# Kernel optimization log

Hardware: AMD Instinct MI355X
Metric: run time of the kernel (lower is better)

The kernel has to match this reference:

```python
import jax, jax.numpy as jnp
import numpy as np

B, DIN, DP, DOUT, K, N = 4, 64, 3, 64, 16, 8192


def setup_inputs() -> dict:
    key = jax.random.key(0)
    ks = jax.random.split(key, 5)
    features = jax.random.normal(ks[0], (B, DIN, N), dtype=jnp.float32)
    positions = jax.random.normal(ks[1], (B, DP, N), dtype=jnp.float32)
    neighborhoods = jax.random.randint(ks[2], (B, K, N), 0, N, dtype=jnp.int32)
    position_theta = jax.random.normal(ks[3], (DP, DIN, DOUT), dtype=jnp.float32) * 0.05
    position_bias = jnp.zeros((DIN, DOUT), dtype=jnp.float32)
    feature_bias = jnp.zeros((DOUT, 1), dtype=jnp.float32)
    return {
        "features": features,
        "positions": positions,
        "neighborhoods": neighborhoods,
        "position_theta": position_theta,
        "position_bias": position_bias,
        "feature_bias": feature_bias,
    }


def _gather_neighbors(x, idx):
    # x: [D, N], idx: [K, N] -> [D, K, N]
    return x[:, idx]


def reference(features, positions, neighborhoods, position_theta, position_bias, feature_bias):
    # Gather neighbor features/positions: [B, D, K, N]
    fg = jax.vmap(_gather_neighbors)(features, neighborhoods)      # [B, Din, K, N]
    pg = jax.vmap(_gather_neighbors)(positions, neighborhoods)     # [B, Dp,  K, N]
    # Relative positions of neighbors w.r.t. center point
    rel = pg - positions[:, :, None, :]                            # [B, Dp, K, N]
    # Dynamic weight w[b,k,n] = theta . rel + bias, contracted with
    # gathered features and summed over K, without materializing [Din,Dout] per neighbor.
    y = jnp.einsum('pio,bpkn,bikn->bon', position_theta, rel, fg)
    y = y + jnp.einsum('io,bikn->bon', position_bias, fg)
    # feature bias [Dout, 1] broadcasts over [B, Dout, N]
    y = y + feature_bias[None, :, :]
    return y  # [B, Dout, N]; activation=None (linear)
```

## Files before the change

kernel.cpp:

```cpp
#include <hip/hip_runtime.h>

#define NB    4
#define DIN_  64
#define DOUT_ 64
#define KN    16
#define NPT   8192
#define CPAD  264

typedef __attribute__((ext_vector_type(8))) short short8;
typedef __attribute__((ext_vector_type(4))) float v4f;

__device__ __forceinline__ float bf2f(unsigned short u) {
    unsigned int x = ((unsigned int)u) << 16;
    float f; __builtin_memcpy(&f, &x, 4); return f;
}
__device__ __forceinline__ unsigned short f2bf(float f) {
    unsigned int x; __builtin_memcpy(&x, &f, 4);
    x += 0x7fffu + ((x >> 16) & 1u);
    return (unsigned short)(x >> 16);
}

__global__ void k_prep(const float* __restrict__ feat, const float* __restrict__ pos,
                       const float* __restrict__ theta, const float* __restrict__ pbias,
                       unsigned short* __restrict__ ft, float4* __restrict__ pt,
                       unsigned short* __restrict__ tbf) {
    __shared__ float tile[64][65];
    const int bid = blockIdx.x;
    if (bid < 512) {
        int b = bid >> 7, n0 = (bid & 127) << 6;
        int lane = threadIdx.x & 63, w = threadIdx.x >> 6;
#pragma unroll
        for (int r = 0; r < 16; ++r) {
            int i = (r << 2) | w;
            tile[i][lane] = feat[(b*DIN_ + i)*NPT + n0 + lane];
        }
        __syncthreads();
#pragma unroll
        for (int r = 0; r < 16; ++r) {
            int n = (r << 2) | w;
            ft[((size_t)(b*NPT + n0 + n))*DIN_ + lane] = f2bf(tile[lane][n]);
        }
    } else if (bid < 640) {
        int t = (bid - 512)*256 + threadIdx.x;
        int b = t >> 13, n = t & 8191;
        float4 v;
        v.x = pos[(b*3 + 0)*NPT + n];
        v.y = pos[(b*3 + 1)*NPT + n];
        v.z = pos[(b*3 + 2)*NPT + n];
        v.w = 1.0f;
        pt[t] = v;
    } else {
        int e = (bid - 640)*256 + threadIdx.x;
        int o = e >> 5, g = e & 31;
        short8 u;
#pragma unroll
        for (int j = 0; j < 8; ++j) {
            int c = g*8 + j;
            float v = (c < 192) ? theta[c*64 + o] : pbias[(c - 192)*64 + o];
            u[j] = (short)f2bf(v);
        }
        *reinterpret_cast<short8*>(tbf + o*256 + g*8) = u;
    }
}

template<bool USE_WS>
__global__ __launch_bounds__(256, 4) void k_main(
    const float*          __restrict__ feat,
    const float*          __restrict__ pos,
    const int*            __restrict__ nbr,
    const float*          __restrict__ theta,
    const float*          __restrict__ pbias,
    const float*          __restrict__ fbias,
    const unsigned short* __restrict__ ft,
    const float4*         __restrict__ pt,
    const unsigned short* __restrict__ tbf,
    float*                __restrict__ out)
{
    __shared__ __align__(16) unsigned short Xt[32*CPAD];
    __shared__ int    nbs[KN*32];
    __shared__ float4 pcs[32];

    const int tid  = threadIdx.x;
    const int lane = tid & 63;
    const int w    = tid >> 6;
    const int j16  = lane & 15;
    const int pt2  = lane >> 4;

    const int base = blockIdx.x << 5;
    const int b    = base >> 13;
    const int nb0  = base & 8191;

#pragma unroll
    for (int r = 0; r < 2; ++r) {
        int idx = tid + (r << 8);
        int k = idx >> 5, c = idx & 31;
        nbs[idx] = nbr[(b*KN + k)*NPT + nb0 + c];
    }
    if (tid < 128) {
        if (USE_WS) {
            ((float*)pcs)[tid] = ((const float*)(pt + b*NPT + nb0))[tid];
        } else if (tid < 32) {
            int n = nb0 + tid;
            pcs[tid] = make_float4(pos[(b*3+0)*NPT + n], pos[(b*3+1)*NPT + n],
                                   pos[(b*3+2)*NPT + n], 1.0f);
        }
    }
    __syncthreads();

    const unsigned short* ftb = ft + (((size_t)b) << 19);

#pragma unroll
    for (int pass = 0; pass < 2; ++pass) {
        const int q = (w << 3) + (pass << 2) + pt2;
        const float4 pc = pcs[q];
        float acc[4][4];
#pragma unroll
        for (int p = 0; p < 4; ++p)
#pragma unroll
            for (int j = 0; j < 4; ++j) acc[p][j] = 0.f;

#pragma unroll 4
        for (int k = 0; k < KN; ++k) {
            const int id = nbs[(k << 5) + q];
            float4 pg; float f[4];
            if (USE_WS) {
                pg = pt[b*NPT + id];
                ushort4 fr = *reinterpret_cast<const ushort4*>(
                    ftb + (((size_t)id) << 6) + (j16 << 2));
                f[0]=bf2f(fr.x); f[1]=bf2f(fr.y); f[2]=bf2f(fr.z); f[3]=bf2f(fr.w);
            } else {
                pg.x = pos[(b*3+0)*NPT + id];
                pg.y = pos[(b*3+1)*NPT + id];
                pg.z = pos[(b*3+2)*NPT + id];
                pg.w = 1.0f;
#pragma unroll
                for (int j = 0; j < 4; ++j)
                    f[j] = feat[(b*DIN_ + (j16<<2) + j)*NPT + id];
            }
#pragma unroll
            for (int j = 0; j < 4; ++j) {
                acc[0][j] += pg.x * f[j];
                acc[1][j] += pg.y * f[j];
                acc[2][j] += pg.z * f[j];
                acc[3][j] += f[j];
            }
        }
#pragma unroll
        for (int j = 0; j < 4; ++j) {
            acc[0][j] -= pc.x * acc[3][j];
            acc[1][j] -= pc.y * acc[3][j];
            acc[2][j] -= pc.z * acc[3][j];
        }
#pragma unroll
        for (int p = 0; p < 4; ++p) {
            ushort4 pk;
            pk.x = f2bf(acc[p][0]); pk.y = f2bf(acc[p][1]);
            pk.z = f2bf(acc[p][2]); pk.w = f2bf(acc[p][3]);
            *reinterpret_cast<ushort4*>(&Xt[q*CPAD + (p<<6) + (j16<<2)]) = pk;
        }
    }
    __syncthreads();

    const int kg   = pt2;
    const int orow = (w << 4) + j16;
    v4f acc0 = {0.f,0.f,0.f,0.f}, acc1 = {0.f,0.f,0.f,0.f};
#pragma unroll
    for (int ks = 0; ks < 8; ++ks) {
        const int koff = (ks << 5) + (kg << 3);
        short8 a;
        if (USE_WS) {
            a = *reinterpret_cast<const short8*>(tbf + orow*256 + koff);
        } else {
#pragma unroll
            for (int j = 0; j < 8; ++j) {
                int c = koff + j;
                float v = (c < 192) ? theta[c*64 + orow] : pbias[(c - 192)*64 + orow];
                a[j] = (short)f2bf(v);
            }
        }
        short8 b0 = *reinterpret_cast<const short8*>(&Xt[j16*CPAD + koff]);
        short8 b1 = *reinterpret_cast<const short8*>(&Xt[(16 + j16)*CPAD + koff]);
        acc0 = __builtin_amdgcn_mfma_f32_16x16x32_bf16(a, b0, acc0, 0, 0, 0);
        acc1 = __builtin_amdgcn_mfma_f32_16x16x32_bf16(a, b1, acc1, 0, 0, 0);
    }
#pragma unroll
    for (int r = 0; r < 4; ++r) {
        const int o = (w << 4) + (kg << 2) + r;
        const float fb = fbias[o];
        const size_t rowoff = (size_t)(b*DOUT_ + o)*NPT + nb0;
        out[rowoff + j16]      = acc0[r] + fb;
        out[rowoff + 16 + j16] = acc1[r] + fb;
    }
}

extern "C" void kernel_launch(void* const* d_in, const int* in_sizes, int n_in,
                              void* d_out, int out_size, void* d_ws, size_t ws_size,
                              hipStream_t stream) {
    const float* feat  = (const float*)d_in[0];
    const float* pos   = (const float*)d_in[1];
    const int*   nbr   = (const int*)d_in[2];
    const float* theta = (const float*)d_in[3];
    const float* pbias = (const float*)d_in[4];
    const float* fbias = (const float*)d_in[5];
    float* out = (float*)d_out;

    const size_t ft_bytes  = (size_t)NB*NPT*DIN_*2;
    const size_t pt_bytes  = (size_t)NB*NPT*sizeof(float4);
    const size_t tbf_bytes = (size_t)DOUT_*256*2;
    const int n_blocks = (NB*NPT)/32;

    if (ws_size >= ft_bytes + pt_bytes + tbf_bytes) {
        unsigned short* ft  = (unsigned short*)d_ws;
        float4*         pt  = (float4*)((char*)d_ws + ft_bytes);
        unsigned short* tbf = (unsigned short*)((char*)d_ws + ft_bytes + pt_bytes);
        k_prep<<<648, 256, 0, stream>>>(feat, pos, theta, pbias, ft, pt, tbf);
        k_main<true><<<n_blocks, 256, 0, stream>>>(feat, pos, nbr, theta, pbias, fbias,
                                                   ft, pt, tbf, out);
    } else {
        k_main<false><<<n_blocks, 256, 0, stream>>>(feat, pos, nbr, theta, pbias, fbias,
                                                    (const unsigned short*)feat,
                                                    (const float4*)feat,
                                                    (const unsigned short*)feat, out);
    }
}
```

Before: 89.25 us.

## Remap gather phase to one pass with 8 channels per lane and direct index loads

The gather/accumulate phase now gives each lane 8 bf16 channels loaded as one 16-byte short8 instead of 4 channels loaded as 8 bytes. With 8 points per wave, the two-pass loop collapses into a single pass. The neighbor indices and center positions are read straight from global memory rather than staged through shared memory. The K loop is fully unrolled, which drops a __syncthreads and exposes more independent loads, at the cost of more registers (a 32-float accumulator) and possibly lower occupancy.

```diff
diff --git a/kernel.cpp b/kernel.cpp
--- a/kernel.cpp
+++ b/kernel.cpp
@@ -77,91 +77,81 @@
     float*                __restrict__ out)
 {
     __shared__ __align__(16) unsigned short Xt[32*CPAD];
-    __shared__ int    nbs[KN*32];
-    __shared__ float4 pcs[32];
 
     const int tid  = threadIdx.x;
     const int lane = tid & 63;
     const int w    = tid >> 6;
-    const int j16  = lane & 15;
-    const int pt2  = lane >> 4;
+    const int j8   = lane & 7;
+    const int pq   = lane >> 3;
 
     const int base = blockIdx.x << 5;
     const int b    = base >> 13;
     const int nb0  = base & 8191;
-
-#pragma unroll
-    for (int r = 0; r < 2; ++r) {
-        int idx = tid + (r << 8);
-        int k = idx >> 5, c = idx & 31;
-        nbs[idx] = nbr[(b*KN + k)*NPT + nb0 + c];
-    }
-    if (tid < 128) {
+    const int q    = (w << 3) + pq;
+    const int n    = nb0 + q;
+
+    const unsigned short* ftb = ft + (((size_t)b) << 19);
+    const float4*         ptb = pt + b*NPT;
+
+    float4 pc;
+    if (USE_WS) pc = ptb[n];
+    else {
+        pc.x = pos[(b*3+0)*NPT + n];
+        pc.y = pos[(b*3+1)*NPT + n];
+        pc.z = pos[(b*3+2)*NPT + n];
+        pc.w = 1.0f;
+    }
+
+    float acc[4][8];
+#pragma unroll
+    for (int p = 0; p < 4; ++p)
+#pragma unroll
+        for (int j = 0; j < 8; ++j) acc[p][j] = 0.f;
+
+#pragma unroll
+    for (int k = 0; k < KN; ++k) {
+        const int id = nbr[(b*KN + k)*NPT + n];
+        float4 pg; float f[8];
         if (USE_WS) {
-            ((float*)pcs)[tid] = ((const float*)(pt + b*NPT + nb0))[tid];
-        } else if (tid < 32) {
-            int n = nb0 + tid;
-            pcs[tid] = make_float4(pos[(b*3+0)*NPT + n], pos[(b*3+1)*NPT + n],
-                                   pos[(b*3+2)*NPT + n], 1.0f);
-        }
+            pg = ptb[id];
+            short8 fr = *reinterpret_cast<const short8*>(
+                ftb + (((size_t)id) << 6) + (j8 << 3));
+#pragma unroll
+            for (int j = 0; j < 8; ++j) f[j] = bf2f((unsigned short)fr[j]);
+        } else {
+            pg.x = pos[(b*3+0)*NPT + id];
+            pg.y = pos[(b*3+1)*NPT + id];
+            pg.z = pos[(b*3+2)*NPT + id];
+            pg.w = 1.0f;
+#pragma unroll
+            for (int j = 0; j < 8; ++j)
+                f[j] = feat[(b*DIN_ + (j8<<3) + j)*NPT + id];
+        }
+#pragma unroll
+        for (int j = 0; j < 8; ++j) {
+            acc[0][j] += pg.x * f[j];
+            acc[1][j] += pg.y * f[j];
+            acc[2][j] += pg.z * f[j];
+            acc[3][j] += f[j];
+        }
+    }
+#pragma unroll
+    for (int j = 0; j < 8; ++j) {
+        acc[0][j] -= pc.x * acc[3][j];
+        acc[1][j] -= pc.y * acc[3][j];
+        acc[2][j] -= pc.z * acc[3][j];
+    }
+#pragma unroll
+    for (int p = 0; p < 4; ++p) {
+        short8 pk;
+#pragma unroll
+        for (int j = 0; j < 8; ++j) pk[j] = (short)f2bf(acc[p][j]);
+        *reinterpret_cast<short8*>(&Xt[q*CPAD + (p<<6) + (j8<<3)]) = pk;
     }
     __syncthreads();
 
-    const unsigned short* ftb = ft + (((size_t)b) << 19);
-
-#pragma unroll
-    for (int pass = 0; pass < 2; ++pass) {
-        const int q = (w << 3) + (pass << 2) + pt2;
-        const float4 pc = pcs[q];
-        float acc[4][4];
-#pragma unroll
-        for (int p = 0; p < 4; ++p)
-#pragma unroll
-            for (int j = 0; j < 4; ++j) acc[p][j] = 0.f;
-
-#pragma unroll 4
-        for (int k = 0; k < KN; ++k) {
-            const int id = nbs[(k << 5) + q];
-            float4 pg; float f[4];
-            if (USE_WS) {
-                pg = pt[b*NPT + id];
-                ushort4 fr = *reinterpret_cast<const ushort4*>(
-                    ftb + (((size_t)id) << 6) + (j16 << 2));
-                f[0]=bf2f(fr.x); f[1]=bf2f(fr.y); f[2]=bf2f(fr.z); f[3]=bf2f(fr.w);
-            } else {
-                pg.x = pos[(b*3+0)*NPT + id];
-                pg.y = pos[(b*3+1)*NPT + id];
-                pg.z = pos[(b*3+2)*NPT + id];
-                pg.w = 1.0f;
-#pragma unroll
-                for (int j = 0; j < 4; ++j)
-                    f[j] = feat[(b*DIN_ + (j16<<2) + j)*NPT + id];
-            }
-#pragma unroll
-            for (int j = 0; j < 4; ++j) {
-                acc[0][j] += pg.x * f[j];
-                acc[1][j] += pg.y * f[j];
-                acc[2][j] += pg.z * f[j];
-                acc[3][j] += f[j];
-            }
-        }
-#pragma unroll
-        for (int j = 0; j < 4; ++j) {
-            acc[0][j] -= pc.x * acc[3][j];
-            acc[1][j] -= pc.y * acc[3][j];
-            acc[2][j] -= pc.z * acc[3][j];
-        }
-#pragma unroll
-        for (int p = 0; p < 4; ++p) {
-            ushort4 pk;
-            pk.x = f2bf(acc[p][0]); pk.y = f2bf(acc[p][1]);
-            pk.z = f2bf(acc[p][2]); pk.w = f2bf(acc[p][3]);
-            *reinterpret_cast<ushort4*>(&Xt[q*CPAD + (p<<6) + (j16<<2)]) = pk;
-        }
-    }
-    __syncthreads();
-
-    const int kg   = pt2;
+    const int j16 = lane & 15;
+    const int kg  = lane >> 4;
     const int orow = (w << 4) + j16;
     v4f acc0 = {0.f,0.f,0.f,0.f}, acc1 = {0.f,0.f,0.f,0.f};
 #pragma unroll
```

Measured after the change: 91.73 us (median of 2 runs). 1.03x slower.
